# Performance work log

Measured on AMD Instinct MI355X. Metric: run time of the kernel, lower is better.

The kernel has to match this reference:

```python
import jax, jax.numpy as jnp
import numpy as np

B, NPTS, NBOX = 16, 100000, 64
PTS_THRESHOLD = 2048          # topk voxels kept per scene
GT_THRESHOLD = 2.5            # distance multiplier
VOXEL_SIZE = 0.01
TENSOR_STRIDE = 8             # stride of the level being pruned
SIZE = TENSOR_STRIDE * VOXEL_SIZE  # 0.08, per-voxel cell size at this level


def setup_inputs() -> dict:
    key = jax.random.key(0)
    k1, k2, k3 = jax.random.split(key, 3)
    scores = jax.random.normal(k1, (B, NPTS), dtype=jnp.float32)
    points = jax.random.uniform(k2, (B, NPTS, 3), dtype=jnp.float32)
    gt_centers = jax.random.uniform(k3, (B, NBOX, 3), dtype=jnp.float32)
    return {"scores": scores, "points": points, "gt_centers": gt_centers}


def reference(scores, points, gt_centers):
    # --- per-batch topk score mask (MEFPN3D._get_score_mask) ---
    _, idx = jax.lax.top_k(scores, PTS_THRESHOLD)          # [B, K]
    score_mask = jnp.zeros(scores.shape, dtype=bool)
    score_mask = score_mask.at[jnp.arange(B)[:, None], idx].set(True)  # scatter True

    # --- gt distance mask (MEFPN3D._get_gt_mask) ---
    # distances: [B, Npts, n_boxes]
    diff = points[:, :, None, :] - gt_centers[:, None, :, :]
    distances = jnp.sqrt(jnp.sum(diff * diff, axis=-1))
    gt_mask = jnp.any(distances < SIZE * GT_THRESHOLD, axis=-1)        # [B, Npts]

    # --- combined prune mask (scatter of per-batch masks into global mask) ---
    prune_mask = jnp.logical_or(score_mask, gt_mask)

    # --- per-voxel sigmoid BCE loss, reduction='none' (CrossEntropyLoss use_sigmoid=True) ---
    target = gt_mask.astype(scores.dtype)
    losses = target * jax.nn.softplus(-scores) + (1.0 - target) * jax.nn.softplus(scores)
    return prune_mask, losses
```

## Files before the change

### kernel.cpp

```cpp
#include <hip/hip_runtime.h>
#include <hip/hip_bf16.h>
#include <stdint.h>

#define BB 16
#define NPTS 100000
#define NBOX 64
#define KTOP 2048
#define THRF 0.2f
#define C_LO 0.039984f
#define C_HI 0.040016f

#define SLICES 16
#define SLICE_SPAN 6272
#define SCAP 512
#define LIST_CAP 4096
#define CUT 0xC0000000u

#define CAND_OFF 0
#define CNT_OFF  (BB * SLICES * SCAP)

__device__ __forceinline__ uint32_t fmap(float f) {
    uint32_t b = __float_as_uint(f);
    return (b & 0x80000000u) ? ~b : (b | 0x80000000u);
}

__global__ __launch_bounds__(256) void cand_k(const float* __restrict__ scores,
                                              uint32_t* __restrict__ ws) {
    __shared__ uint32_t buf[SCAP];
    __shared__ uint32_t lcnt;
    const int b = blockIdx.y, sl = blockIdx.x, tid = threadIdx.x;
    if (tid == 0) lcnt = 0;
    __syncthreads();
    const int start = sl * SLICE_SPAN;
    const int nf4 = min(SLICE_SPAN, NPTS - start) >> 2;
    const float4* sc4 = reinterpret_cast<const float4*>(scores + (size_t)b * NPTS + start);
    for (int i4 = tid; i4 < nf4; i4 += 256) {
        const float4 v = sc4[i4];
        const uint32_t u[4] = {fmap(v.x), fmap(v.y), fmap(v.z), fmap(v.w)};
#pragma unroll
        for (int j = 0; j < 4; ++j) {
            if (u[j] >= CUT) {
                const uint32_t pos = atomicAdd(&lcnt, 1u);
                if (pos < SCAP) buf[pos] = u[j];
            }
        }
    }
    __syncthreads();
    const uint32_t c = lcnt;
    uint32_t* dst = ws + CAND_OFF + ((size_t)(b * SLICES + sl)) * SCAP;
    const uint32_t cw = c < SCAP ? c : SCAP;
    for (uint32_t i = tid; i < cw; i += 256) dst[i] = buf[i];
    if (tid == 0) ws[CNT_OFF + b * SLICES + sl] = c;
}

__device__ __forceinline__ void pick256(const uint32_t* __restrict__ hist,
                                        uint32_t* __restrict__ excl,
                                        int tid, int lane, uint32_t target,
                                        uint32_t* sBin, uint32_t* sKrem,
                                        uint32_t* sE, uint32_t* sTot, int wantE) {
    __syncthreads();
    if (tid < 64) {
        const uint32_t v0 = hist[4*tid], v1 = hist[4*tid+1], v2 = hist[4*tid+2], v3 = hist[4*tid+3];
        const uint32_t lt = v0 + v1 + v2 + v3;
        uint32_t x = lt;
#pragma unroll
        for (int off = 1; off < 64; off <<= 1) {
            const uint32_t y = __shfl_up(x, off);
            if (lane >= off) x += y;
        }
        const uint32_t ex = x - lt;
        excl[4*tid] = ex; excl[4*tid+1] = ex + v0;
        excl[4*tid+2] = ex + v0 + v1; excl[4*tid+3] = ex + v0 + v1 + v2;
        if (tid == 63) *sTot = x;
    }
    __syncthreads();
    {
        const uint32_t total = *sTot, lim = total - target;
        const uint32_t pe = excl[tid];
        const uint32_t pe1 = (tid == 255) ? total : excl[tid + 1];
        if (pe <= lim && pe1 > lim) {
            *sBin = (uint32_t)tid;
            *sKrem = target - (total - pe1);
            if (wantE) *sE = pe1 - pe;
        }
    }
    __syncthreads();
}

__device__ __noinline__ bool exact_gt(float px, float py, float pz,
                                      const float* __restrict__ C) {
    bool hit = false;
#pragma unroll 1
    for (int k = 0; k < NBOX; ++k) {
        float dx = px - C[3 * k + 0];
        float dy = py - C[3 * k + 1];
        float dz = pz - C[3 * k + 2];
        float d2 = __fadd_rn(__fadd_rn(__fmul_rn(dx, dx), __fmul_rn(dy, dy)),
                             __fmul_rn(dz, dz));
        if (__fsqrt_rn(d2) < THRF) hit = true;
    }
    return hit;
}

__global__ __launch_bounds__(256) void main_k(const float* __restrict__ scores,
                                              const float* __restrict__ points,
                                              const float* __restrict__ ctrs,
                                              const uint32_t* __restrict__ ws,
                                              float* __restrict__ out) {
    const int b = blockIdx.y, tid = threadIdx.x, w = tid >> 6, lane = tid & 63;
    __shared__ float4 sbox[NBOX];
    __shared__ uint32_t list[LIST_CAP];
    __shared__ uint32_t h4[4][257];
    __shared__ uint32_t hist[256], excl[256];
    __shared__ uint32_t scnt[SLICES], soff[SLICES];
    __shared__ uint32_t wcnt[4];
    __shared__ uint32_t sBin, sKrem, sE, sTot, sIstar, sRun, sSpec, sUni, lcnt;

    const float* sc = scores + (size_t)b * NPTS;
    const float* C = ctrs + b * NBOX * 3;

    if (tid < NBOX) {
        const float cx = C[3 * tid], cy = C[3 * tid + 1], cz = C[3 * tid + 2];
        sbox[tid] = make_float4(-2.0f * cx, -2.0f * cy, -2.0f * cz,
                                fmaf(cx, cx, fmaf(cy, cy, cz * cz)));
    }

    if (tid < SLICES) scnt[tid] = ws[CNT_OFF + b * SLICES + tid];
    __syncthreads();
    if (tid == 0) {
        uint32_t tot = 0; bool ok = true;
        for (int s = 0; s < SLICES; ++s) {
            soff[s] = tot;
            const uint32_t c = scnt[s];
            if (c > SCAP) ok = false;
            tot += c;
        }
        sTot = tot;
        sSpec = (ok && tot >= KTOP && tot <= LIST_CAP) ? 1u : 0u;
        sKrem = KTOP;
        sIstar = NPTS;
        lcnt = 0;
        sUni = 1u;
    }
    __syncthreads();

    uint32_t cnt, prefix = 0u;
    int shift0;
    if (sSpec) {
        cnt = sTot;
#pragma unroll 1
        for (int s = 0; s < SLICES; ++s) {
            const uint32_t c = scnt[s], o = soff[s];
            const uint32_t* src = ws + CAND_OFF + ((size_t)(b * SLICES + s)) * SCAP;
            for (uint32_t i = tid; i < c; i += 256) list[o + i] = src[i];
        }
        __syncthreads();
        const uint32_t b0 = list[0] >> 24;
        bool uni = true;
        for (uint32_t i = tid; i < cnt; i += 256) uni &= ((list[i] >> 24) == b0);
        if (!uni) atomicAnd(&sUni, 0u);
        __syncthreads();
        if (sUni) { prefix = b0 << 24; shift0 = 16; }
        else      { prefix = 0u;       shift0 = 24; }
    } else {
        for (int i = tid; i < 4 * 257; i += 256) (&h4[0][0])[i] = 0;
        __syncthreads();
        const float4* sc4 = reinterpret_cast<const float4*>(sc);
        for (int i4 = tid; i4 < NPTS / 4; i4 += 256) {
            const float4 v = sc4[i4];
            atomicAdd(&h4[w][fmap(v.x) >> 24], 1u);
            atomicAdd(&h4[w][fmap(v.y) >> 24], 1u);
            atomicAdd(&h4[w][fmap(v.z) >> 24], 1u);
            atomicAdd(&h4[w][fmap(v.w) >> 24], 1u);
        }
        __syncthreads();
        hist[tid] = h4[0][tid] + h4[1][tid] + h4[2][tid] + h4[3][tid];
        pick256(hist, excl, tid, lane, KTOP, &sBin, &sKrem, &sE, &sTot, 0);
        const uint32_t beta = sBin;
        for (int i4 = tid; i4 < NPTS / 4; i4 += 256) {
            const float4 v = sc4[i4];
            const uint32_t u[4] = {fmap(v.x), fmap(v.y), fmap(v.z), fmap(v.w)};
#pragma unroll
            for (int j = 0; j < 4; ++j) {
                if ((u[j] >> 24) == beta) {
                    const uint32_t pos = atomicAdd(&lcnt, 1u);
                    if (pos < LIST_CAP) list[pos] = u[j];
                }
            }
        }
        __syncthreads();
        cnt = lcnt < LIST_CAP ? lcnt : LIST_CAP;
        prefix = beta << 24;
        shift0 = 16;
    }

#pragma unroll 1
    for (int shift = shift0; shift >= 0; shift -= 8) {
        for (int i = tid; i < 4 * 257; i += 256) (&h4[0][0])[i] = 0;
        __syncthreads();
        const uint32_t hi8 = (shift < 24) ? (prefix >> (shift + 8)) : 0u;
        uint32_t* mh = h4[lane & 3];
        for (uint32_t i = tid; i < cnt; i += 256) {
            const uint32_t uu = list[i];
            const bool m = (shift == 24) || ((uu >> (shift + 8)) == hi8);
            if (m) atomicAdd(&mh[(uu >> shift) & 255u], 1u);
        }
        __syncthreads();
        hist[tid] = h4[0][tid] + h4[1][tid] + h4[2][tid] + h4[3][tid];
        const uint32_t target = sKrem;
        pick256(hist, excl, tid, lane, target, &sBin, &sKrem, &sE, &sTot,
                shift == 0 ? 1 : 0);
        prefix |= sBin << shift;
    }

    const uint32_t R = sKrem, E = sE;
    const uint32_t tbits = (prefix & 0x80000000u) ? (prefix & 0x7fffffffu) : ~prefix;

    if (E != R) {
        const float T = __uint_as_float(tbits);
        if (tid == 0) sRun = 0;
        __syncthreads();
        for (int base = 0; base < NPTS; base += 256) {
            const uint32_t r0 = sRun;
            if (r0 > R) break;
            const int i = base + tid;
            const bool eq = (i < NPTS) && (sc[i] == T);
            const unsigned long long mask = __ballot(eq);
            if (lane == 0) wcnt[w] = (uint32_t)__popcll(mask);
            __syncthreads();
            uint32_t before = 0, total = 0;
#pragma unroll
            for (int ww = 0; ww < 4; ++ww) {
                const uint32_t c = wcnt[ww];
                if (ww < w) before += c;
                total += c;
            }
            if (eq) {
                const uint32_t rank = r0 + before +
                    (uint32_t)__popcll(mask & ((1ull << lane) - 1ull));
                if (rank == R) sIstar = (uint32_t)i;
            }
            __syncthreads();
            if (tid == 0) sRun = r0 + total;
            __syncthreads();
        }
    }
    __syncthreads();
    const float T = __uint_as_float(tbits);
    const uint32_t Istar = sIstar;

    const int p0 = blockIdx.x * 1024 + tid * 4;
    if (p0 >= NPTS) return;

    const float* P = points + ((size_t)b * NPTS + p0) * 3;
    const float4 a = *reinterpret_cast<const float4*>(P);
    const float4 c4 = *reinterpret_cast<const float4*>(P + 4);
    const float4 e = *reinterpret_cast<const float4*>(P + 8);
    const float px[4] = {a.x, a.w, c4.z, e.y};
    const float py[4] = {a.y, c4.x, c4.w, e.z};
    const float pz[4] = {a.z, c4.y, e.x, e.w};
    float m2[4] = {1e30f, 1e30f, 1e30f, 1e30f};

#pragma unroll 8
    for (int k = 0; k < NBOX; ++k) {
        const float4 B = sbox[k];
#pragma unroll
        for (int j = 0; j < 4; ++j) {
            const float t = fmaf(B.x, px[j], fmaf(B.y, py[j], fmaf(B.z, pz[j], B.w)));
            m2[j] = fminf(m2[j], t);
        }
    }

    const float4 sv = *reinterpret_cast<const float4*>(sc + p0);
    const float s[4] = {sv.x, sv.y, sv.z, sv.w};
    float pr[4], ls[4];
#pragma unroll
    for (int j = 0; j < 4; ++j) {
        const float pp = fmaf(px[j], px[j], fmaf(py[j], py[j], pz[j] * pz[j]));
        const float m = pp + m2[j];
        bool gt;
        if (m < C_LO) gt = true;
        else if (m >= C_HI) gt = false;
        else gt = exact_gt(px[j], py[j], pz[j], C);
        const bool sm = (s[j] > T) || (s[j] == T && (uint32_t)(p0 + j) < Istar);
        pr[j] = (gt || sm) ? 1.0f : 0.0f;
        const float x = gt ? -s[j] : s[j];
        ls[j] = fmaxf(x, 0.0f) + __logf(1.0f + __expf(-fabsf(s[j])));
    }
    float* o0 = out + (size_t)b * NPTS + p0;
    float* o1 = out + (size_t)BB * NPTS + (size_t)b * NPTS + p0;
    *reinterpret_cast<float4*>(o0) = make_float4(pr[0], pr[1], pr[2], pr[3]);
    *reinterpret_cast<float4*>(o1) = make_float4(ls[0], ls[1], ls[2], ls[3]);
}

extern "C" void kernel_launch(void* const* d_in, const int* in_sizes, int n_in,
                              void* d_out, int out_size, void* d_ws, size_t ws_size,
                              hipStream_t stream) {
    const float* scores = (const float*)d_in[0];
    const float* points = (const float*)d_in[1];
    const float* ctrs   = (const float*)d_in[2];
    float* out = (float*)d_out;
    uint32_t* ws = (uint32_t*)d_ws;

    const dim3 gridC(SLICES, BB);
    cand_k<<<gridC, 256, 0, stream>>>(scores, ws);
    const dim3 gridP(98, BB);
    main_k<<<gridP, 256, 0, stream>>>(scores, points, ctrs, ws, out);
}
```

Measured before the change: 51.19 us.

## Compute top-k threshold once per batch in separate kernel instead of per block

Moves the per-batch top-k threshold selection and box precomputation out of main_k into a new selfin_k kernel launched with one block per batch, storing the threshold, tie index and transformed boxes in workspace. main_k then just reads these values, eliminating redundant selection work repeated by every block and reducing its shared memory footprint. Adds an extra kernel launch and a serialized dependency with only 16 blocks active during selection. Also tweaks unroll factors.

```diff
diff --git a/kernel.cpp b/kernel.cpp
--- a/kernel.cpp
+++ b/kernel.cpp
@@ -18,6 +18,8 @@
 
 #define CAND_OFF 0
 #define CNT_OFF  (BB * SLICES * SCAP)
+#define STATE_OFF (CNT_OFF + BB * SLICES)
+#define TBOX_OFF  (STATE_OFF + BB * 2)
 
 __device__ __forceinline__ uint32_t fmap(float f) {
     uint32_t b = __float_as_uint(f);
@@ -87,28 +89,10 @@
     __syncthreads();
 }
 
-__device__ __noinline__ bool exact_gt(float px, float py, float pz,
-                                      const float* __restrict__ C) {
-    bool hit = false;
-#pragma unroll 1
-    for (int k = 0; k < NBOX; ++k) {
-        float dx = px - C[3 * k + 0];
-        float dy = py - C[3 * k + 1];
-        float dz = pz - C[3 * k + 2];
-        float d2 = __fadd_rn(__fadd_rn(__fmul_rn(dx, dx), __fmul_rn(dy, dy)),
-                             __fmul_rn(dz, dz));
-        if (__fsqrt_rn(d2) < THRF) hit = true;
-    }
-    return hit;
-}
-
-__global__ __launch_bounds__(256) void main_k(const float* __restrict__ scores,
-                                              const float* __restrict__ points,
-                                              const float* __restrict__ ctrs,
-                                              const uint32_t* __restrict__ ws,
-                                              float* __restrict__ out) {
-    const int b = blockIdx.y, tid = threadIdx.x, w = tid >> 6, lane = tid & 63;
-    __shared__ float4 sbox[NBOX];
+__global__ __launch_bounds__(256) void selfin_k(const float* __restrict__ scores,
+                                                const float* __restrict__ ctrs,
+                                                uint32_t* __restrict__ ws) {
+    const int b = blockIdx.x, tid = threadIdx.x, w = tid >> 6, lane = tid & 63;
     __shared__ uint32_t list[LIST_CAP];
     __shared__ uint32_t h4[4][257];
     __shared__ uint32_t hist[256], excl[256];
@@ -117,12 +101,14 @@
     __shared__ uint32_t sBin, sKrem, sE, sTot, sIstar, sRun, sSpec, sUni, lcnt;
 
     const float* sc = scores + (size_t)b * NPTS;
-    const float* C = ctrs + b * NBOX * 3;
 
     if (tid < NBOX) {
-        const float cx = C[3 * tid], cy = C[3 * tid + 1], cz = C[3 * tid + 2];
-        sbox[tid] = make_float4(-2.0f * cx, -2.0f * cy, -2.0f * cz,
-                                fmaf(cx, cx, fmaf(cy, cy, cz * cz)));
+        const float cx = ctrs[(size_t)b * NBOX * 3 + 3 * tid];
+        const float cy = ctrs[(size_t)b * NBOX * 3 + 3 * tid + 1];
+        const float cz = ctrs[(size_t)b * NBOX * 3 + 3 * tid + 2];
+        float4* TB = reinterpret_cast<float4*>(ws + TBOX_OFF) + b * NBOX;
+        TB[tid] = make_float4(-2.0f * cx, -2.0f * cy, -2.0f * cz,
+                              fmaf(cx, cx, fmaf(cy, cy, cz * cz)));
     }
 
     if (tid < SLICES) scnt[tid] = ws[CNT_OFF + b * SLICES + tid];
@@ -148,7 +134,7 @@
     int shift0;
     if (sSpec) {
         cnt = sTot;
-#pragma unroll 1
+#pragma unroll 2
         for (int s = 0; s < SLICES; ++s) {
             const uint32_t c = scnt[s], o = soff[s];
             const uint32_t* src = ws + CAND_OFF + ((size_t)(b * SLICES + s)) * SCAP;
@@ -244,10 +230,41 @@
             if (tid == 0) sRun = r0 + total;
             __syncthreads();
         }
-    }
-    __syncthreads();
-    const float T = __uint_as_float(tbits);
-    const uint32_t Istar = sIstar;
+        __syncthreads();
+    }
+    if (tid == 0) {
+        uint32_t* st = ws + STATE_OFF + b * 2;
+        st[0] = tbits;
+        st[1] = sIstar;
+    }
+}
+
+__device__ __noinline__ bool exact_gt(float px, float py, float pz,
+                                      const float* __restrict__ C) {
+    bool hit = false;
+#pragma unroll 1
+    for (int k = 0; k < NBOX; ++k) {
+        float dx = px - C[3 * k + 0];
+        float dy = py - C[3 * k + 1];
+        float dz = pz - C[3 * k + 2];
+        float d2 = __fadd_rn(__fadd_rn(__fmul_rn(dx, dx), __fmul_rn(dy, dy)),
+                             __fmul_rn(dz, dz));
+        if (__fsqrt_rn(d2) < THRF) hit = true;
+    }
+    return hit;
+}
+
+__global__ __launch_bounds__(256) void main_k(const float* __restrict__ scores,
+                                              const float* __restrict__ points,
+                                              const float* __restrict__ ctrs,
+                                              const uint32_t* __restrict__ ws,
+                                              float* __restrict__ out) {
+    const int b = blockIdx.y, tid = threadIdx.x;
+    const uint32_t* st = ws + STATE_OFF + b * 2;
+    const float T = __uint_as_float(st[0]);
+    const uint32_t Istar = st[1];
+    const float4* __restrict__ TB =
+        reinterpret_cast<const float4*>(ws + TBOX_OFF) + b * NBOX;
 
     const int p0 = blockIdx.x * 1024 + tid * 4;
     if (p0 >= NPTS) return;
@@ -261,9 +278,9 @@
     const float pz[4] = {a.z, c4.y, e.x, e.w};
     float m2[4] = {1e30f, 1e30f, 1e30f, 1e30f};
 
-#pragma unroll 8
+#pragma unroll 16
     for (int k = 0; k < NBOX; ++k) {
-        const float4 B = sbox[k];
+        const float4 B = TB[k];
 #pragma unroll
         for (int j = 0; j < 4; ++j) {
             const float t = fmaf(B.x, px[j], fmaf(B.y, py[j], fmaf(B.z, pz[j], B.w)));
@@ -271,7 +288,7 @@
         }
     }
 
-    const float4 sv = *reinterpret_cast<const float4*>(sc + p0);
+    const float4 sv = *reinterpret_cast<const float4*>(scores + (size_t)b * NPTS + p0);
     const float s[4] = {sv.x, sv.y, sv.z, sv.w};
     float pr[4], ls[4];
 #pragma unroll
@@ -281,7 +298,7 @@
         bool gt;
         if (m < C_LO) gt = true;
         else if (m >= C_HI) gt = false;
-        else gt = exact_gt(px[j], py[j], pz[j], C);
+        else gt = exact_gt(px[j], py[j], pz[j], ctrs + b * NBOX * 3);
         const bool sm = (s[j] > T) || (s[j] == T && (uint32_t)(p0 + j) < Istar);
         pr[j] = (gt || sm) ? 1.0f : 0.0f;
         const float x = gt ? -s[j] : s[j];
@@ -304,6 +321,7 @@
 
     const dim3 gridC(SLICES, BB);
     cand_k<<<gridC, 256, 0, stream>>>(scores, ws);
+    selfin_k<<<BB, 256, 0, stream>>>(scores, ctrs, ws);
     const dim3 gridP(98, BB);
     main_k<<<gridP, 256, 0, stream>>>(scores, points, ctrs, ws, out);
 }
```

After: 49.38 us. -3.5%, faster.
